# Optimization experiments

Measured on AMD Instinct MI355X. Metric: run time of the kernel, lower is better.

## Reference

```python
import jax, jax.numpy as jnp
import numpy as np

T, INPUT, RES = 8192, 1024, 4096


def setup_inputs() -> dict:
    key = jax.random.key(0)
    k1, k2, k3 = jax.random.split(key, 3)
    x = jax.random.normal(k1, (T, INPUT, 1), dtype=jnp.float32)
    # nn.init.uniform_(a=-1, b=1)
    W_in = jax.random.uniform(k2, (RES, INPUT), dtype=jnp.float32, minval=-1.0, maxval=1.0)
    # diagonal of W_res: uniform(-spectral_radius, spectral_radius), spectral_radius=1.0
    d = jax.random.uniform(k3, (RES,), dtype=jnp.float32, minval=-1.0, maxval=1.0)
    return {"x": x, "W_in": W_in, "d": d}


def reference(x, W_in, d):
    # Precompute input projection for all timesteps: [T, RES]
    # (the per-step W_in @ x_t hoisted out of the sequential loop)
    U = jnp.einsum('ri,ti->tr', W_in, x[:, :, 0])

    # W_res is diagonal, so W_res @ state == d * state (elementwise).
    def step(s, u):
        s_new = jnp.tanh(u + d * s)
        return s_new, s_new

    s0 = jnp.zeros((RES,), dtype=x.dtype)  # initial state (torch.zeros)
    _, states = jax.lax.scan(step, s0, U)  # states: [T, RES]
    return states[:, :, None]  # torch.unsqueeze(states, -1) -> [T, RES, 1]
```

## Files before the change

kernel.cpp:

```cpp
#include <hip/hip_runtime.h>
#include <hip/hip_bf16.h>

#define T_DIM 8192
#define IN_DIM 1024
#define RES_DIM 4096

typedef unsigned short u16;
typedef _Float16 f16;
typedef f16 f16x8 __attribute__((ext_vector_type(8)));
typedef float f32x4 __attribute__((ext_vector_type(4)));
typedef float f32x16 __attribute__((ext_vector_type(16)));

__device__ __forceinline__ float tanh_fast(float z) {
    z = fminf(15.0f, fmaxf(-15.0f, z));
    float e = __expf(2.0f * z);
    float inv = __builtin_amdgcn_rcpf(e + 1.0f);
    return fmaf(-2.0f, inv, 1.0f);
}

__device__ __forceinline__ void stage16(const u16* g, u16* l) {
    __builtin_amdgcn_global_load_lds(
        (const __attribute__((address_space(1))) void*)g,
        (__attribute__((address_space(3))) void*)l, 16, 0, 0);
}

__global__ void convert_f16_pair(const float* __restrict__ src, u16* __restrict__ hi,
                                 u16* __restrict__ lo, int nchunks) {
    for (int c = blockIdx.x * blockDim.x + threadIdx.x; c < nchunks;
         c += gridDim.x * blockDim.x) {
        int row = c & 127;
        int kq  = (c >> 7) & 3;
        int kt  = (c >> 9) & 31;
        int rt  = c >> 14;
        const float* s = src + (size_t)(rt * 128 + row) * 1024 + kt * 32 + kq * 8;
        float4 f0 = *(const float4*)s;
        float4 f1 = *(const float4*)(s + 4);
        float f[8] = {f0.x, f0.y, f0.z, f0.w, f1.x, f1.y, f1.z, f1.w};
        alignas(16) u16 hv[8];
        alignas(16) u16 lv[8];
#pragma unroll
        for (int e = 0; e < 8; ++e) {
            f16 h = (f16)f[e];
            f16 l = (f16)(f[e] - (float)h);
            hv[e] = *(const u16*)&h;
            lv[e] = *(const u16*)&l;
        }
        *(uint4*)(hi + (size_t)c * 8) = *(const uint4*)hv;
        *(uint4*)(lo + (size_t)c * 8) = *(const uint4*)lv;
    }
}

__global__ void convert_f16_single(const float* __restrict__ src, u16* __restrict__ dst,
                                   int nchunks) {
    for (int c = blockIdx.x * blockDim.x + threadIdx.x; c < nchunks;
         c += gridDim.x * blockDim.x) {
        int row = c & 127;
        int kq  = (c >> 7) & 3;
        int kt  = (c >> 9) & 31;
        int rt  = c >> 14;
        const float* s = src + (size_t)(rt * 128 + row) * 1024 + kt * 32 + kq * 8;
        float4 f0 = *(const float4*)s;
        float4 f1 = *(const float4*)(s + 4);
        float f[8] = {f0.x, f0.y, f0.z, f0.w, f1.x, f1.y, f1.z, f1.w};
        alignas(16) u16 hv[8];
#pragma unroll
        for (int e = 0; e < 8; ++e) {
            f16 h = (f16)f[e];
            hv[e] = *(const u16*)&h;
        }
        *(uint4*)(dst + (size_t)c * 8) = *(const uint4*)hv;
    }
}

__global__ __launch_bounds__(256)
void gemm_f16_wide(const u16* __restrict__ Xh, const u16* __restrict__ Xl,
                   const u16* __restrict__ Wf, float* __restrict__ C) {
    __shared__ __attribute__((aligned(16))) u16 sAh[4096];
    __shared__ __attribute__((aligned(16))) u16 sAl[4096];
    __shared__ __attribute__((aligned(16))) u16 sW[2][4096];

    const int tid  = threadIdx.x;
    const int lane = tid & 63;
    const int wave = tid >> 6;
    const int wr = wave >> 1, wc = wave & 1;
    const int bm = blockIdx.x, bn = blockIdx.y;

    f32x16 acc[2][4] = {};

    const int l31 = lane & 31;
    const int kgl = lane >> 5;

    for (int kt = 0; kt < 32; ++kt) {
        const u16* gX0 = Xh + ((size_t)(bm * 32 + kt)) * 4096;
        const u16* gX1 = Xl + ((size_t)(bm * 32 + kt)) * 4096;
        const u16* gW0 = Wf + ((size_t)((bn * 2 + 0) * 32 + kt)) * 4096;
        const u16* gW1 = Wf + ((size_t)((bn * 2 + 1) * 32 + kt)) * 4096;
        __syncthreads();
#pragma unroll
        for (int i = 0; i < 2; ++i) {
            int off = i * 2048 + tid * 8;
            int wb  = i * 2048 + (tid & ~63) * 8;
            stage16(gX0 + off, sAh + wb);
            stage16(gX1 + off, sAl + wb);
            stage16(gW0 + off, &sW[0][0] + wb);
            stage16(gW1 + off, &sW[1][0] + wb);
        }
        __syncthreads();

        f16x8 ah[2][2], al8[2][2], bw[4][2];
#pragma unroll
        for (int mf = 0; mf < 2; ++mf)
#pragma unroll
            for (int ks = 0; ks < 2; ++ks) {
                int ao = (ks * 2 + kgl) * 1024 + (wr * 64 + mf * 32 + l31) * 8;
                ah[mf][ks]  = *(const f16x8*)(sAh + ao);
                al8[mf][ks] = *(const f16x8*)(sAl + ao);
            }
#pragma unroll
        for (int nf = 0; nf < 4; ++nf)
#pragma unroll
            for (int ks = 0; ks < 2; ++ks) {
                int bo = (ks * 2 + kgl) * 1024 + (nf * 32 + l31) * 8;
                bw[nf][ks] = *(const f16x8*)(&sW[wc][0] + bo);
            }
#pragma unroll
        for (int mf = 0; mf < 2; ++mf)
#pragma unroll
            for (int nf = 0; nf < 4; ++nf)
#pragma unroll
                for (int ks = 0; ks < 2; ++ks) {
                    acc[mf][nf] = __builtin_amdgcn_mfma_f32_32x32x16_f16(
                        ah[mf][ks], bw[nf][ks], acc[mf][nf], 0, 0, 0);
                    acc[mf][nf] = __builtin_amdgcn_mfma_f32_32x32x16_f16(
                        al8[mf][ks], bw[nf][ks], acc[mf][nf], 0, 0, 0);
                }
    }

    const size_t t0 = (size_t)bm * 128 + wr * 64;
    const size_t c0 = (size_t)bn * 256 + wc * 128;
#pragma unroll
    for (int mf = 0; mf < 2; ++mf)
#pragma unroll
        for (int nf = 0; nf < 4; ++nf) {
            float* cp = C + (t0 + mf * 32) * RES_DIM + (c0 + nf * 32 + l31);
#pragma unroll
            for (int r = 0; r < 16; ++r) {
                int row = (r & 3) + 8 * (r >> 2) + 4 * kgl;
                cp[(size_t)row * RES_DIM] = acc[mf][nf][r];
            }
        }
}

__global__ __launch_bounds__(256)
void gemm_f32(const float* __restrict__ A, const float* __restrict__ B, float* __restrict__ C) {
    __shared__ float sAf[64][33];
    __shared__ float sBf[64][33];
    const int tid = threadIdx.x;
    const int tx = tid & 15, ty = tid >> 4;
    const size_t t0 = (size_t)blockIdx.x * 64;
    const size_t r0 = (size_t)blockIdx.y * 64;
    const int lrow = tid >> 2;
    const int lcol = (tid & 3) * 8;
    float acc[4][4] = {};
    for (int k0 = 0; k0 < IN_DIM; k0 += 32) {
        float4 a0 = *(const float4*)&A[(t0 + lrow) * IN_DIM + k0 + lcol];
        float4 a1 = *(const float4*)&A[(t0 + lrow) * IN_DIM + k0 + lcol + 4];
        float4 b0 = *(const float4*)&B[(r0 + lrow) * IN_DIM + k0 + lcol];
        float4 b1 = *(const float4*)&B[(r0 + lrow) * IN_DIM + k0 + lcol + 4];
        __syncthreads();
        sAf[lrow][lcol + 0] = a0.x; sAf[lrow][lcol + 1] = a0.y;
        sAf[lrow][lcol + 2] = a0.z; sAf[lrow][lcol + 3] = a0.w;
        sAf[lrow][lcol + 4] = a1.x; sAf[lrow][lcol + 5] = a1.y;
        sAf[lrow][lcol + 6] = a1.z; sAf[lrow][lcol + 7] = a1.w;
        sBf[lrow][lcol + 0] = b0.x; sBf[lrow][lcol + 1] = b0.y;
        sBf[lrow][lcol + 2] = b0.z; sBf[lrow][lcol + 3] = b0.w;
        sBf[lrow][lcol + 4] = b1.x; sBf[lrow][lcol + 5] = b1.y;
        sBf[lrow][lcol + 6] = b1.z; sBf[lrow][lcol + 7] = b1.w;
        __syncthreads();
#pragma unroll
        for (int kk = 0; kk < 32; ++kk) {
            float av[4], bv[4];
#pragma unroll
            for (int i = 0; i < 4; ++i) av[i] = sAf[ty * 4 + i][kk];
#pragma unroll
            for (int j = 0; j < 4; ++j) bv[j] = sBf[tx * 4 + j][kk];
#pragma unroll
            for (int i = 0; i < 4; ++i)
#pragma unroll
                for (int j = 0; j < 4; ++j) acc[i][j] = fmaf(av[i], bv[j], acc[i][j]);
        }
    }
#pragma unroll
    for (int i = 0; i < 4; ++i)
#pragma unroll
        for (int j = 0; j < 4; ++j)
            C[(t0 + ty * 4 + i) * RES_DIM + r0 + tx * 4 + j] = acc[i][j];
}

__global__ void warmup2_kernel(const float* __restrict__ U, const float* __restrict__ d,
                               float* __restrict__ sinit, int C, int W, int NC) {
    int g = blockIdx.x * blockDim.x + threadIdx.x;
    if (g >= NC * (RES_DIM / 2)) return;
    int c = g >> 11;
    int r2 = g & 2047;
    float2 s = make_float2(0.0f, 0.0f);
    if (c > 0) {
        float2 dr = ((const float2*)d)[r2];
        const float2* p = (const float2*)U + (size_t)(c * C - W) * 2048 + r2;
        constexpr int PF = 8;
        float2 buf[PF];
#pragma unroll
        for (int i = 0; i < PF; ++i) buf[i] = p[(size_t)i * 2048];
        for (int t = 0; t < W; t += PF) {
#pragma unroll
            for (int j = 0; j < PF; ++j) {
                float2 u = buf[j];
                int tn = t + j + PF;
                if (tn < W) buf[j] = p[(size_t)tn * 2048];
                s.x = tanh_fast(fmaf(dr.x, s.x, u.x));
                s.y = tanh_fast(fmaf(dr.y, s.y, u.y));
            }
        }
    }
    ((float2*)sinit)[g] = s;
}

__global__ void scan2_kernel(float* __restrict__ U, const float* __restrict__ d,
                             const float* __restrict__ sinit, int C, int NC) {
    int g = blockIdx.x * blockDim.x + threadIdx.x;
    if (g >= NC * (RES_DIM / 2)) return;
    int c = g >> 11;
    int r2 = g & 2047;
    float2 dr = ((const float2*)d)[r2];
    float2 s = (c == 0) ? make_float2(0.0f, 0.0f) : ((const float2*)sinit)[g];
    float2* p = (float2*)U + (size_t)c * C * 2048 + r2;
    constexpr int PF = 8;
    float2 buf[PF];
#pragma unroll
    for (int i = 0; i < PF; ++i) buf[i] = p[(size_t)i * 2048];
    for (int t = 0; t < C; t += PF) {
#pragma unroll
        for (int j = 0; j < PF; ++j) {
            float2 u = buf[j];
            int tn = t + j + PF;
            if (tn < C) buf[j] = p[(size_t)tn * 2048];
            s.x = tanh_fast(fmaf(dr.x, s.x, u.x));
            s.y = tanh_fast(fmaf(dr.y, s.y, u.y));
            p[(size_t)(t + j) * 2048] = s;
        }
    }
}

extern "C" void kernel_launch(void* const* d_in, const int* in_sizes, int n_in,
                              void* d_out, int out_size, void* d_ws, size_t ws_size,
                              hipStream_t stream) {
    const float* x    = (const float*)d_in[0];
    const float* W_in = (const float*)d_in[1];
    const float* dvec = (const float*)d_in[2];
    float* out = (float*)d_out;

    constexpr int NC   = 64;
    constexpr int CHK  = T_DIM / NC;
    constexpr int WARM = 64;

    const size_t szX = (size_t)T_DIM * IN_DIM * sizeof(u16);
    const size_t szW = (size_t)RES_DIM * IN_DIM * sizeof(u16);
    const size_t szS = (size_t)NC * RES_DIM * sizeof(float);

    if (ws_size >= 2 * szX + szW + szS) {
        u16* Xh = (u16*)d_ws;
        u16* Xl = Xh + (size_t)T_DIM * IN_DIM;
        u16* Wf = Xl + (size_t)T_DIM * IN_DIM;
        float* sinit = (float*)(Wf + (size_t)RES_DIM * IN_DIM);

        convert_f16_pair<<<2048, 256, 0, stream>>>(x, Xh, Xl, T_DIM * IN_DIM / 8);
        convert_f16_single<<<1024, 256, 0, stream>>>(W_in, Wf, RES_DIM * IN_DIM / 8);
        gemm_f16_wide<<<dim3(T_DIM / 128, RES_DIM / 256), 256, 0, stream>>>(Xh, Xl, Wf, out);
        warmup2_kernel<<<NC * (RES_DIM / 2) / 256, 256, 0, stream>>>(out, dvec, sinit, CHK, WARM, NC);
        scan2_kernel<<<NC * (RES_DIM / 2) / 256, 256, 0, stream>>>(out, dvec, sinit, CHK, NC);
    } else {
        gemm_f32<<<dim3(T_DIM / 64, RES_DIM / 64), 256, 0, stream>>>(x, W_in, out);
        if (ws_size >= szS) {
            float* sinit = (float*)d_ws;
            warmup2_kernel<<<NC * (RES_DIM / 2) / 256, 256, 0, stream>>>(out, dvec, sinit, CHK, WARM, NC);
            scan2_kernel<<<NC * (RES_DIM / 2) / 256, 256, 0, stream>>>(out, dvec, sinit, CHK, NC);
        } else {
            scan2_kernel<<<(RES_DIM / 2) / 256, 256, 0, stream>>>(out, dvec, nullptr, T_DIM, 1);
        }
    }
}
```

Baseline: 205.1 us.

## Merge conversion kernels and stage two K-tiles per barrier in GEMM

Combines the x hi/lo split and W_in f16 conversion into one launch, removing a kernel launch and its tail. The GEMM now loads two K-tiles per sync pair into doubled shared buffers (64 KB), halving the number of barriers and issuing more loads at once. This doubles LDS use, which may limit occupancy despite the launch_bounds min-blocks hint of 2. Loads and compute within each pair are still not overlapped.

```diff
diff --git a/kernel.cpp b/kernel.cpp
--- a/kernel.cpp
+++ b/kernel.cpp
@@ -24,17 +24,20 @@
         (__attribute__((address_space(3))) void*)l, 16, 0, 0);
 }
 
-__global__ void convert_f16_pair(const float* __restrict__ src, u16* __restrict__ hi,
-                                 u16* __restrict__ lo, int nchunks) {
-    for (int c = blockIdx.x * blockDim.x + threadIdx.x; c < nchunks;
-         c += gridDim.x * blockDim.x) {
+__global__ void convert_all(const float* __restrict__ x, const float* __restrict__ Wsrc,
+                            u16* __restrict__ Xh, u16* __restrict__ Xl,
+                            u16* __restrict__ Wf, int nX, int nTot) {
+    for (int g = blockIdx.x * blockDim.x + threadIdx.x; g < nTot;
+         g += gridDim.x * blockDim.x) {
+        const int isX = (g < nX);
+        const int c   = isX ? g : (g - nX);
         int row = c & 127;
         int kq  = (c >> 7) & 3;
         int kt  = (c >> 9) & 31;
         int rt  = c >> 14;
-        const float* s = src + (size_t)(rt * 128 + row) * 1024 + kt * 32 + kq * 8;
-        float4 f0 = *(const float4*)s;
-        float4 f1 = *(const float4*)(s + 4);
+        const float* src = (isX ? x : Wsrc) + (size_t)(rt * 128 + row) * 1024 + kt * 32 + kq * 8;
+        float4 f0 = *(const float4*)src;
+        float4 f1 = *(const float4*)(src + 4);
         float f[8] = {f0.x, f0.y, f0.z, f0.w, f1.x, f1.y, f1.z, f1.w};
         alignas(16) u16 hv[8];
         alignas(16) u16 lv[8];
@@ -45,39 +48,21 @@
             hv[e] = *(const u16*)&h;
             lv[e] = *(const u16*)&l;
         }
-        *(uint4*)(hi + (size_t)c * 8) = *(const uint4*)hv;
-        *(uint4*)(lo + (size_t)c * 8) = *(const uint4*)lv;
-    }
-}
-
-__global__ void convert_f16_single(const float* __restrict__ src, u16* __restrict__ dst,
-                                   int nchunks) {
-    for (int c = blockIdx.x * blockDim.x + threadIdx.x; c < nchunks;
-         c += gridDim.x * blockDim.x) {
-        int row = c & 127;
-        int kq  = (c >> 7) & 3;
-        int kt  = (c >> 9) & 31;
-        int rt  = c >> 14;
-        const float* s = src + (size_t)(rt * 128 + row) * 1024 + kt * 32 + kq * 8;
-        float4 f0 = *(const float4*)s;
-        float4 f1 = *(const float4*)(s + 4);
-        float f[8] = {f0.x, f0.y, f0.z, f0.w, f1.x, f1.y, f1.z, f1.w};
-        alignas(16) u16 hv[8];
-#pragma unroll
-        for (int e = 0; e < 8; ++e) {
-            f16 h = (f16)f[e];
-            hv[e] = *(const u16*)&h;
-        }
-        *(uint4*)(dst + (size_t)c * 8) = *(const uint4*)hv;
-    }
-}
-
-__global__ __launch_bounds__(256)
-void gemm_f16_wide(const u16* __restrict__ Xh, const u16* __restrict__ Xl,
-                   const u16* __restrict__ Wf, float* __restrict__ C) {
-    __shared__ __attribute__((aligned(16))) u16 sAh[4096];
-    __shared__ __attribute__((aligned(16))) u16 sAl[4096];
-    __shared__ __attribute__((aligned(16))) u16 sW[2][4096];
+        if (isX) {
+            *(uint4*)(Xh + (size_t)c * 8) = *(const uint4*)hv;
+            *(uint4*)(Xl + (size_t)c * 8) = *(const uint4*)lv;
+        } else {
+            *(uint4*)(Wf + (size_t)c * 8) = *(const uint4*)hv;
+        }
+    }
+}
+
+__global__ __launch_bounds__(256, 2)
+void gemm_f16_wide2(const u16* __restrict__ Xh, const u16* __restrict__ Xl,
+                    const u16* __restrict__ Wf, float* __restrict__ C) {
+    __shared__ __attribute__((aligned(16))) u16 sAh[2][4096];
+    __shared__ __attribute__((aligned(16))) u16 sAl[2][4096];
+    __shared__ __attribute__((aligned(16))) u16 sW[2][2][4096];
 
     const int tid  = threadIdx.x;
     const int lane = tid & 63;
@@ -90,50 +75,57 @@
     const int l31 = lane & 31;
     const int kgl = lane >> 5;
 
-    for (int kt = 0; kt < 32; ++kt) {
-        const u16* gX0 = Xh + ((size_t)(bm * 32 + kt)) * 4096;
-        const u16* gX1 = Xl + ((size_t)(bm * 32 + kt)) * 4096;
-        const u16* gW0 = Wf + ((size_t)((bn * 2 + 0) * 32 + kt)) * 4096;
-        const u16* gW1 = Wf + ((size_t)((bn * 2 + 1) * 32 + kt)) * 4096;
-        __syncthreads();
-#pragma unroll
-        for (int i = 0; i < 2; ++i) {
-            int off = i * 2048 + tid * 8;
-            int wb  = i * 2048 + (tid & ~63) * 8;
-            stage16(gX0 + off, sAh + wb);
-            stage16(gX1 + off, sAl + wb);
-            stage16(gW0 + off, &sW[0][0] + wb);
-            stage16(gW1 + off, &sW[1][0] + wb);
-        }
-        __syncthreads();
-
-        f16x8 ah[2][2], al8[2][2], bw[4][2];
-#pragma unroll
-        for (int mf = 0; mf < 2; ++mf)
-#pragma unroll
-            for (int ks = 0; ks < 2; ++ks) {
-                int ao = (ks * 2 + kgl) * 1024 + (wr * 64 + mf * 32 + l31) * 8;
-                ah[mf][ks]  = *(const f16x8*)(sAh + ao);
-                al8[mf][ks] = *(const f16x8*)(sAl + ao);
+    for (int ktp = 0; ktp < 16; ++ktp) {
+        __syncthreads();
+#pragma unroll
+        for (int s = 0; s < 2; ++s) {
+            const int kt = ktp * 2 + s;
+            const u16* gX0 = Xh + ((size_t)(bm * 32 + kt)) * 4096;
+            const u16* gX1 = Xl + ((size_t)(bm * 32 + kt)) * 4096;
+            const u16* gW0 = Wf + ((size_t)((bn * 2 + 0) * 32 + kt)) * 4096;
+            const u16* gW1 = Wf + ((size_t)((bn * 2 + 1) * 32 + kt)) * 4096;
+#pragma unroll
+            for (int i = 0; i < 2; ++i) {
+                int off = i * 2048 + tid * 8;
+                int wb  = i * 2048 + (tid & ~63) * 8;
+                stage16(gX0 + off, &sAh[s][0] + wb);
+                stage16(gX1 + off, &sAl[s][0] + wb);
+                stage16(gW0 + off, &sW[s][0][0] + wb);
+                stage16(gW1 + off, &sW[s][1][0] + wb);
             }
-#pragma unroll
-        for (int nf = 0; nf < 4; ++nf)
-#pragma unroll
-            for (int ks = 0; ks < 2; ++ks) {
-                int bo = (ks * 2 + kgl) * 1024 + (nf * 32 + l31) * 8;
-                bw[nf][ks] = *(const f16x8*)(&sW[wc][0] + bo);
-            }
-#pragma unroll
-        for (int mf = 0; mf < 2; ++mf)
+        }
+        __syncthreads();
+
+#pragma unroll
+        for (int s = 0; s < 2; ++s) {
+            f16x8 ah[2][2], al8[2][2], bw[4][2];
+#pragma unroll
+            for (int mf = 0; mf < 2; ++mf)
+#pragma unroll
+                for (int ks = 0; ks < 2; ++ks) {
+                    int ao = (ks * 2 + kgl) * 1024 + (wr * 64 + mf * 32 + l31) * 8;
+                    ah[mf][ks]  = *(const f16x8*)(&sAh[s][0] + ao);
+                    al8[mf][ks] = *(const f16x8*)(&sAl[s][0] + ao);
+                }
 #pragma unroll
             for (int nf = 0; nf < 4; ++nf)
 #pragma unroll
                 for (int ks = 0; ks < 2; ++ks) {
-                    acc[mf][nf] = __builtin_amdgcn_mfma_f32_32x32x16_f16(
-                        ah[mf][ks], bw[nf][ks], acc[mf][nf], 0, 0, 0);
-                    acc[mf][nf] = __builtin_amdgcn_mfma_f32_32x32x16_f16(
-                        al8[mf][ks], bw[nf][ks], acc[mf][nf], 0, 0, 0);
+                    int bo = (ks * 2 + kgl) * 1024 + (nf * 32 + l31) * 8;
+                    bw[nf][ks] = *(const f16x8*)(&sW[s][wc][0] + bo);
                 }
+#pragma unroll
+            for (int mf = 0; mf < 2; ++mf)
+#pragma unroll
+                for (int nf = 0; nf < 4; ++nf)
+#pragma unroll
+                    for (int ks = 0; ks < 2; ++ks) {
+                        acc[mf][nf] = __builtin_amdgcn_mfma_f32_32x32x16_f16(
+                            ah[mf][ks], bw[nf][ks], acc[mf][nf], 0, 0, 0);
+                        acc[mf][nf] = __builtin_amdgcn_mfma_f32_32x32x16_f16(
+                            al8[mf][ks], bw[nf][ks], acc[mf][nf], 0, 0, 0);
+                    }
+        }
     }
 
     const size_t t0 = (size_t)bm * 128 + wr * 64;
@@ -273,9 +265,10 @@
         u16* Wf = Xl + (size_t)T_DIM * IN_DIM;
         float* sinit = (float*)(Wf + (size_t)RES_DIM * IN_DIM);
 
-        convert_f16_pair<<<2048, 256, 0, stream>>>(x, Xh, Xl, T_DIM * IN_DIM / 8);
-        convert_f16_single<<<1024, 256, 0, stream>>>(W_in, Wf, RES_DIM * IN_DIM / 8);
-        gemm_f16_wide<<<dim3(T_DIM / 128, RES_DIM / 256), 256, 0, stream>>>(Xh, Xl, Wf, out);
+        const int nX   = T_DIM * IN_DIM / 8;
+        const int nTot = nX + RES_DIM * IN_DIM / 8;
+        convert_all<<<3072, 256, 0, stream>>>(x, W_in, Xh, Xl, Wf, nX, nTot);
+        gemm_f16_wide2<<<dim3(T_DIM / 128, RES_DIM / 256), 256, 0, stream>>>(Xh, Xl, Wf, out);
         warmup2_kernel<<<NC * (RES_DIM / 2) / 256, 256, 0, stream>>>(out, dvec, sinit, CHK, WARM, NC);
         scan2_kernel<<<NC * (RES_DIM / 2) / 256, 256, 0, stream>>>(out, dvec, sinit, CHK, NC);
     } else {
```

Measured after the change: 205.9 us. No clear change (+0.4%).
